# Kernel optimization log

Measured on AMD Instinct MI355X. Metric: run time of the kernel, lower is better.

The kernel has to match this reference:

```python
import jax, jax.numpy as jnp
import numpy as np

B, NC, H, GH = 64, 21, 32, 64  # batch, num_class, hidden spatial, geo spatial
DN = ('NCHW', 'OIHW', 'NCHW')


def conv2d(x, w, b, stride, pad):
    y = jax.lax.conv_general_dilated(x, w, (stride, stride), [(pad, pad), (pad, pad)], dimension_numbers=DN)
    return y + b[None, :, None, None]


def group_norm(x, scale, bias, groups=32, eps=1e-5):
    b, c, h, w = x.shape
    xg = x.reshape(b, groups, c // groups, h, w)
    mean = xg.mean(axis=(2, 3, 4), keepdims=True)
    var = xg.var(axis=(2, 3, 4), keepdims=True)
    xn = ((xg - mean) * jax.lax.rsqrt(var + eps)).reshape(b, c, h, w)
    return xn * scale[None, :, None, None] + bias[None, :, None, None]


def setup_inputs() -> dict:
    key = jax.random.key(0)
    ks = iter(jax.random.split(key, 64))
    rn = lambda shape, s=0.05: jax.random.normal(next(ks), shape, jnp.float32) * s
    inp = {
        'hidden_state': jnp.tanh(rn((B, 128, H, H), 1.0)),
        'delta_flow': rn((B, 2, H, H), 1.0),
        'mask': jax.random.uniform(next(ks), (B, 1, H, H), jnp.float32),
        'geo': rn((B, 8, GH, GH), 1.0),
        'obj_id': jax.random.randint(next(ks), (B,), 1, NC + 1),
        # geo_model
        'g1_w': rn((128, 8, 3, 3)), 'g1_b': rn((128,)),
        'g2_w': rn((64, 128, 3, 3)), 'g2_b': rn((64,)),
        # delta_flow_model
        'd1_w': rn((128, 2, 7, 7)), 'd1_b': rn((128,)),
        'd2_w': rn((64, 128, 3, 3)), 'd2_b': rn((64,)),
        # mask_model
        'm1_w': rn((64, 1, 3, 3)), 'm1_b': rn((64,)),
        'm2_w': rn((32, 64, 3, 3)), 'm2_b': rn((32,)),
        # conv_layers (conv + GroupNorm(32) x3, all stride 2)
        'c1_w': rn((128, 288, 3, 3)), 'c1_b': rn((128,)), 'gn1_s': jnp.ones((128,)), 'gn1_bb': jnp.zeros((128,)),
        'c2_w': rn((128, 128, 3, 3)), 'c2_b': rn((128,)), 'gn2_s': jnp.ones((128,)), 'gn2_bb': jnp.zeros((128,)),
        'c3_w': rn((128, 128, 3, 3)), 'c3_b': rn((128,)), 'gn3_s': jnp.ones((128,)), 'gn3_bb': jnp.zeros((128,)),
        # fc_layers
        'fc1_w': rn((1024, 2048)), 'fc1_b': rn((1024,)),
        'fc2_w': rn((256, 1024)), 'fc2_b': rn((256,)),
        # prediction heads (random instead of zero-init so grads are non-trivial)
        'rot_w': rn((6 * NC, 256)), 'rot_b': jnp.tile(jnp.array([1., 0., 0., 0., 1., 0.], jnp.float32), NC),
        'tr_w': rn((3 * NC, 256)), 'tr_b': rn((3 * NC,)),
    }
    return inp


def reference(hidden_state, delta_flow, mask, geo, obj_id,
              g1_w, g1_b, g2_w, g2_b, d1_w, d1_b, d2_w, d2_b, m1_w, m1_b, m2_w, m2_b,
              c1_w, c1_b, gn1_s, gn1_bb, c2_w, c2_b, gn2_s, gn2_bb, c3_w, c3_b, gn3_s, gn3_bb,
              fc1_w, fc1_b, fc2_w, fc2_b, rot_w, rot_b, tr_w, tr_b):
    relu = jax.nn.relu
    geo_enc = relu(conv2d(relu(conv2d(geo, g1_w, g1_b, 1, 1)), g2_w, g2_b, 2, 1))        # [B,64,32,32]
    df_enc = relu(conv2d(relu(conv2d(delta_flow, d1_w, d1_b, 1, 3)), d2_w, d2_b, 1, 1))  # [B,64,32,32]
    m_enc = relu(conv2d(relu(conv2d(mask, m1_w, m1_b, 1, 1)), m2_w, m2_b, 1, 1))         # [B,32,32,32]
    enc = jnp.concatenate([hidden_state, df_enc, m_enc, geo_enc], axis=1)                # [B,288,32,32]
    x = relu(group_norm(conv2d(enc, c1_w, c1_b, 2, 1), gn1_s, gn1_bb))                   # [B,128,16,16]
    x = relu(group_norm(conv2d(x, c2_w, c2_b, 2, 1), gn2_s, gn2_bb))                     # [B,128,8,8]
    x = relu(group_norm(conv2d(x, c3_w, c3_b, 2, 1), gn3_s, gn3_bb))                     # [B,128,4,4]
    x = x.reshape(x.shape[0], -1)                                                        # [B,2048]
    x = relu(x @ fc1_w.T + fc1_b)
    x = relu(x @ fc2_w.T + fc2_b)                                                        # [B,256]
    tr = (x @ tr_w.T + tr_b).reshape(-1, NC, 3)
    rot = (x @ rot_w.T + rot_b).reshape(-1, NC, 6)
    # torch.index_select(., dim=1, index=obj_id-1)[:, 0, :] -> uses obj_id[0]
    tr = jnp.take(tr, obj_id - 1, axis=1)[:, 0, :]
    rot = jnp.take(rot, obj_id - 1, axis=1)[:, 0, :]
    return (rot, tr)
```

## Files before the change

kernel.cpp:

```cpp
#include <hip/hip_runtime.h>
#include <hip/hip_bf16.h>

typedef __bf16 bf16x8 __attribute__((ext_vector_type(8)));
typedef __bf16 bf16x4 __attribute__((ext_vector_type(4)));
typedef float  f32x4  __attribute__((ext_vector_type(4)));

struct PackArgs {
    const float* src[11];
    __bf16* dst[11];
    int Cout[11], Cin[11], KHW[11], KW[11], Cinpad[11], Kpad[11], mode[11];
    int cum[12];
};

__device__ void pack_dev(const PackArgs& pa, int gidx)
{
    if (gidx >= pa.cum[11]) return;
    int s = 0;
    for (int i = 1; i <= 10; ++i) s += (gidx >= pa.cum[i]) ? 1 : 0;
    int l = gidx - pa.cum[s];
    int Kp = pa.Kpad[s];
    int co = l / Kp, k = l - co * Kp;
    float v = 0.f;
    if (co < pa.Cout[s]) {
        if (pa.mode[s] == 0) {
            int cip = pa.Cinpad[s];
            int tap = k / cip, ci = k - tap * cip;
            if (tap < pa.KHW[s] && ci < pa.Cin[s])
                v = pa.src[s][((long)co * pa.Cin[s] + ci) * pa.KHW[s] + tap];
        } else if (pa.mode[s] == 1) {
            int pix = k >> 7, c = k & 127;
            v = pa.src[s][(long)co * 2048 + c * 16 + pix];
        } else if (pa.mode[s] == 2) {
            v = pa.src[s][(long)co * Kp + k];
        } else {
            int kh = k >> 4, r = k & 15, kw = r >> 1, ci = r & 1;
            if (kh < 7 && kw < 7)
                v = pa.src[s][((long)(co * 2 + ci) * 7 + kh) * 7 + kw];
        }
    }
    pa.dst[s][l] = (__bf16)v;
}

__device__ void pad_nhwc8_dev(const float* __restrict__ in, __bf16* __restrict__ out,
                              int C, int log2HW, long idx)
{
    int c = idx & 7;
    long pixb = idx >> 3;
    long b = pixb >> log2HW;
    long pix = pixb & ((1 << log2HW) - 1);
    float v = 0.f;
    if (c < C) v = in[((b * C + c) << log2HW) + pix];
    out[idx] = (__bf16)v;
}

__device__ void pad_dflow_dev(const float* __restrict__ in, __bf16* __restrict__ out, int idx)
{
    if (idx >= 64 * 40 * 40 * 2) return;
    int c = idx & 1;
    int t = idx >> 1;
    int x = t % 40;
    int t2 = t / 40;
    int y = t2 % 40;
    int b = t2 / 40;
    int hi = y - 3, wi = x - 3;
    float v = 0.f;
    if ((unsigned)hi < 32u && (unsigned)wi < 32u)
        v = in[((long)(b * 2 + c) * 32 + hi) * 32 + wi];
    out[idx] = (__bf16)v;
}

__device__ void hid_dev(const float* __restrict__ h, __bf16* __restrict__ enc, int blk, int tid)
{
    __shared__ float t[32][65];
    int b = blk >> 6;
    int inner = blk & 63;
    int ct = inner & 3, pt = inner >> 2;
    int c0 = ct * 32, p0 = pt * 64;
    int cl = tid >> 6, pl = tid & 63;
#pragma unroll
    for (int i = 0; i < 8; ++i)
        t[cl + i * 4][pl] = h[((long)(b * 128 + c0 + cl + i * 4)) * 1024 + p0 + pl];
    __syncthreads();
    int cc = tid & 31, p2 = tid >> 5;
#pragma unroll
    for (int i = 0; i < 8; ++i)
        enc[((long)b * 1024 + p0 + p2 + i * 8) * 288 + c0 + cc] = (__bf16)t[cc][p2 + i * 8];
}

#define PACK_B 12544
#define GEOPAD_B 8192
#define DF_B 800
#define MASK_B 2048
#define HID_B 4096
#define ZERO_B 80
__global__ __launch_bounds__(256) void prep_kern(PackArgs pa,
    const float* __restrict__ geo, __bf16* __restrict__ geo_p,
    const float* __restrict__ dflow, __bf16* __restrict__ dflow_pp,
    const float* __restrict__ mask, __bf16* __restrict__ mask_p,
    const float* __restrict__ hidden, __bf16* __restrict__ enc,
    float* __restrict__ fc1acc, float* __restrict__ fc2acc)
{
    int blk = blockIdx.x, tid = threadIdx.x;
    if (blk < PACK_B) { pack_dev(pa, blk * 256 + tid); return; }
    blk -= PACK_B;
    if (blk < GEOPAD_B) { pad_nhwc8_dev(geo, geo_p, 8, 12, (long)blk * 256 + tid); return; }
    blk -= GEOPAD_B;
    if (blk < DF_B) { pad_dflow_dev(dflow, dflow_pp, blk * 256 + tid); return; }
    blk -= DF_B;
    if (blk < MASK_B) { pad_nhwc8_dev(mask, mask_p, 1, 10, (long)blk * 256 + tid); return; }
    blk -= MASK_B;
    if (blk < HID_B) { hid_dev(hidden, enc, blk, tid); return; }
    blk -= HID_B;
    long zi = (long)blk * 256 + tid;
    f32x4 z = {};
    if (zi < 16384) *(f32x4*)&fc1acc[zi * 4] = z;
    else { zi -= 16384; *(f32x4*)&fc2acc[zi * 4] = z; }
}

struct ConvGeom {
    int CinTot;
    int Hin, Win;
    int log2HWout, log2Wout;
    int stride, pad;
    int Kpad;
    int KHW;
    int Cout, CTOT, C0;
    int b0i, b0o;
};

template<int BM, int BN, int BK, int THREADS, int WMW, int WNW, int CINPAD, int KW, int MODE, bool OUTBF, bool RELU>
__device__ __forceinline__ void conv_dev2(char* __restrict__ smem_, int bx,
    const __bf16* __restrict__ in_, const __bf16* __restrict__ A,
    const float* __restrict__ bias, void* __restrict__ out_, const ConvGeom& g)
{
    constexpr int MEXT = BM / WMW;
    constexpr int NEXT = BN / WNW;
    constexpr int MFRAG = MEXT / 16;
    constexpr int NFRAG = NEXT / 16;
    constexpr int KROW = BK / 8;
    constexpr int SROWS = THREADS / KROW;
    constexpr int APASS = BM / SROWS;
    constexpr int BPASS = BN / SROWS;
    constexpr int LDK = BK + 8;

    auto As = reinterpret_cast<__bf16 (*)[LDK]>(smem_);
    auto Bs = reinterpret_cast<__bf16 (*)[LDK]>(smem_ + (size_t)BM * LDK * sizeof(__bf16));

    const int tid = threadIdx.x;
    const int ntile = bx * BN;
    const int lane = tid & 63, w = tid >> 6;
    const int wm = (w / WNW) * MEXT, wn = (w % WNW) * NEXT;
    const int lr = lane & 15, lk = (lane >> 4) * 8;
    const int srow = tid / KROW, scol = (tid % KROW) * 8;

    long nbase[BPASS]; int hi0a[BPASS], wi0a[BPASS];
#pragma unroll
    for (int j = 0; j < BPASS; ++j) {
        int n = ntile + j * SROWS + srow;
        int bb = g.b0i + (n >> g.log2HWout);
        int pix = n & ((1 << g.log2HWout) - 1);
        int ho = pix >> g.log2Wout, wo = pix & ((1 << g.log2Wout) - 1);
        hi0a[j] = ho * g.stride - g.pad;
        wi0a[j] = wo * g.stride - g.pad;
        nbase[j] = (((long)bb * g.Hin + hi0a[j]) * g.Win + wi0a[j]) * g.CinTot;
    }

    bf16x8 av[APASS], bv[BPASS];
    auto LOAD = [&](int k0) {
        int k = k0 + scol;
#pragma unroll
        for (int ja = 0; ja < APASS; ++ja)
            av[ja] = *(const bf16x8*)&A[(long)(ja * SROWS + srow) * g.Kpad + k];
        if (MODE == 1) {
            int q = k >> 3;
            int off = (q >> 1) * (g.Win * g.CinTot) + (q & 1) * 8;
#pragma unroll
            for (int j = 0; j < BPASS; ++j)
                bv[j] = *(const bf16x8*)&in_[nbase[j] + off];
        } else {
            int tap = k / CINPAD;
            int ci  = k - tap * CINPAD;
            int kh  = tap / KW;
            int kw  = tap - kh * KW;
            bool tv = tap < g.KHW;
            int off = (kh * g.Win + kw) * g.CinTot + ci;
#pragma unroll
            for (int j = 0; j < BPASS; ++j) {
                bf16x8 z = {};
                int hi = hi0a[j] + kh, wi = wi0a[j] + kw;
                if (tv && (unsigned)hi < (unsigned)g.Hin && (unsigned)wi < (unsigned)g.Win)
                    z = *(const bf16x8*)&in_[nbase[j] + off];
                bv[j] = z;
            }
        }
    };

    f32x4 acc[MFRAG][NFRAG] = {};
    LOAD(0);
    for (int k0 = 0;;) {
        if (k0) __syncthreads();
#pragma unroll
        for (int ja = 0; ja < APASS; ++ja)
            *(bf16x8*)&As[ja * SROWS + srow][scol] = av[ja];
#pragma unroll
        for (int j = 0; j < BPASS; ++j)
            *(bf16x8*)&Bs[j * SROWS + srow][scol] = bv[j];
        __syncthreads();
        int kn = k0 + BK;
        bool more = kn < g.Kpad;
        if (more) LOAD(kn);
#pragma unroll
        for (int kk = 0; kk < BK; kk += 32) {
            bf16x8 bfr[NFRAG], afr[MFRAG];
#pragma unroll
            for (int jn = 0; jn < NFRAG; ++jn)
                bfr[jn] = *(const bf16x8*)&Bs[wn + jn * 16 + lr][kk + lk];
#pragma unroll
            for (int i = 0; i < MFRAG; ++i)
                afr[i] = *(const bf16x8*)&As[wm + i * 16 + lr][kk + lk];
#pragma unroll
            for (int i = 0; i < MFRAG; ++i)
#pragma unroll
                for (int jn = 0; jn < NFRAG; ++jn)
                    acc[i][jn] = __builtin_amdgcn_mfma_f32_16x16x32_bf16(afr[i], bfr[jn], acc[i][jn], 0, 0, 0);
        }
        if (!more) break;
        k0 = kn;
    }

    const int HWm1 = (1 << g.log2HWout) - 1;
#pragma unroll
    for (int i = 0; i < MFRAG; ++i) {
        int co = wm + i * 16 + (lane >> 4) * 4;
        if (co >= g.Cout) continue;
        f32x4 bv4 = *(const f32x4*)&bias[co];
#pragma unroll
        for (int jn = 0; jn < NFRAG; ++jn) {
            int nn = ntile + wn + jn * 16 + lr;
            f32x4 v = acc[i][jn] + bv4;
            if (RELU) { v.x = fmaxf(v.x, 0.f); v.y = fmaxf(v.y, 0.f); v.z = fmaxf(v.z, 0.f); v.w = fmaxf(v.w, 0.f); }
            int ob = nn >> g.log2HWout, opix = nn & HWm1;
            long o = (((long)(g.b0o + ob) << g.log2HWout) + opix) * g.CTOT + g.C0 + co;
            if (OUTBF) {
                bf16x4 o4 = { (__bf16)v.x, (__bf16)v.y, (__bf16)v.z, (__bf16)v.w };
                *(bf16x4*)&((__bf16*)out_)[o] = o4;
            } else {
                *(f32x4*)&((float*)out_)[o] = v;
            }
        }
    }
}

template<int BM, int BN, int BK, int THREADS, int CINPAD, int KW, int MODE, bool OUTBF, bool RELU>
__device__ __forceinline__ void conv_dev(char* __restrict__ smem_, int bx,
    const __bf16* __restrict__ in_, const __bf16* __restrict__ A,
    const float* __restrict__ bias, void* __restrict__ out_, const ConvGeom& g)
{
    constexpr int WAVES = THREADS / 64;
    constexpr int WN = BN / 32;
    constexpr int WM = WAVES / WN;
    constexpr int MEXT = BM / WM;
    constexpr int MFRAG = MEXT / 16;
    constexpr int KROW = BK / 8;
    constexpr int SROWS = THREADS / KROW;
    constexpr int APASS = BM / SROWS;
    constexpr int BPASS = BN / SROWS;

    auto As = reinterpret_cast<__bf16 (*)[BK + 8]>(smem_);
    auto Bs = reinterpret_cast<__bf16 (*)[BK + 8]>(smem_ + (size_t)BM * (BK + 8) * sizeof(__bf16));

    const int tid = threadIdx.x;
    const int ntile = bx * BN;
    const int lane = tid & 63, w = tid >> 6;
    const int wm = (w / WN) * MEXT, wn = (w % WN) * 32;
    const int lr = lane & 15, lk = (lane >> 4) * 8;
    const int srow = tid / KROW, scol = (tid % KROW) * 8;

    long nbase[BPASS]; int hi0a[BPASS], wi0a[BPASS];
#pragma unroll
    for (int j = 0; j < BPASS; ++j) {
        int n = ntile + j * SROWS + srow;
        int bb = g.b0i + (n >> g.log2HWout);
        int pix = n & ((1 << g.log2HWout) - 1);
        int ho = pix >> g.log2Wout, wo = pix & ((1 << g.log2Wout) - 1);
        hi0a[j] = ho * g.stride - g.pad;
        wi0a[j] = wo * g.stride - g.pad;
        nbase[j] = (((long)bb * g.Hin + hi0a[j]) * g.Win + wi0a[j]) * g.CinTot;
    }

    bf16x8 av[APASS], bv[BPASS];
    auto LOAD = [&](int k0) {
        int k = k0 + scol;
#pragma unroll
        for (int ja = 0; ja < APASS; ++ja)
            av[ja] = *(const bf16x8*)&A[(long)(ja * SROWS + srow) * g.Kpad + k];
        if (MODE == 1) {
            int q = k >> 3;
            int off = (q >> 1) * (g.Win * g.CinTot) + (q & 1) * 8;
#pragma unroll
            for (int j = 0; j < BPASS; ++j)
                bv[j] = *(const bf16x8*)&in_[nbase[j] + off];
        } else {
            int tap = k / CINPAD;
            int ci  = k - tap * CINPAD;
            int kh  = tap / KW;
            int kw  = tap - kh * KW;
            bool tv = tap < g.KHW;
            int off = (kh * g.Win + kw) * g.CinTot + ci;
#pragma unroll
            for (int j = 0; j < BPASS; ++j) {
                bf16x8 z = {};
                int hi = hi0a[j] + kh, wi = wi0a[j] + kw;
                if (tv && (unsigned)hi < (unsigned)g.Hin && (unsigned)wi < (unsigned)g.Win)
                    z = *(const bf16x8*)&in_[nbase[j] + off];
                bv[j] = z;
            }
        }
    };

    f32x4 acc[MFRAG][2] = {};
    LOAD(0);
    for (int k0 = 0;;) {
        if (k0) __syncthreads();
#pragma unroll
        for (int ja = 0; ja < APASS; ++ja)
            *(bf16x8*)&As[ja * SROWS + srow][scol] = av[ja];
#pragma unroll
        for (int j = 0; j < BPASS; ++j)
            *(bf16x8*)&Bs[j * SROWS + srow][scol] = bv[j];
        __syncthreads();
        int kn = k0 + BK;
        bool more = kn < g.Kpad;
        if (more) LOAD(kn);
#pragma unroll
        for (int kk = 0; kk < BK; kk += 32) {
            bf16x8 bfr[2];
            bfr[0] = *(const bf16x8*)&Bs[wn + lr][kk + lk];
            bfr[1] = *(const bf16x8*)&Bs[wn + 16 + lr][kk + lk];
#pragma unroll
            for (int i = 0; i < MFRAG; ++i) {
                bf16x8 a = *(const bf16x8*)&As[wm + i * 16 + lr][kk + lk];
                acc[i][0] = __builtin_amdgcn_mfma_f32_16x16x32_bf16(a, bfr[0], acc[i][0], 0, 0, 0);
                acc[i][1] = __builtin_amdgcn_mfma_f32_16x16x32_bf16(a, bfr[1], acc[i][1], 0, 0, 0);
            }
        }
        if (!more) break;
        k0 = kn;
    }

    const int HWm1 = (1 << g.log2HWout) - 1;
#pragma unroll
    for (int i = 0; i < MFRAG; ++i) {
        int co = wm + i * 16 + (lane >> 4) * 4;
        if (co >= g.Cout) continue;
        f32x4 bv4 = *(const f32x4*)&bias[co];
#pragma unroll
        for (int jb = 0; jb < 2; ++jb) {
            int nn = ntile + wn + jb * 16 + lr;
            f32x4 v = acc[i][jb] + bv4;
            if (RELU) { v.x = fmaxf(v.x, 0.f); v.y = fmaxf(v.y, 0.f); v.z = fmaxf(v.z, 0.f); v.w = fmaxf(v.w, 0.f); }
            int ob = nn >> g.log2HWout, opix = nn & HWm1;
            long o = (((long)(g.b0o + ob) << g.log2HWout) + opix) * g.CTOT + g.C0 + co;
            if (OUTBF) {
                bf16x4 o4 = { (__bf16)v.x, (__bf16)v.y, (__bf16)v.z, (__bf16)v.w };
                *(bf16x4*)&((__bf16*)out_)[o] = o4;
            } else {
                *(f32x4*)&((float*)out_)[o] = v;
            }
        }
    }
}

template<int BM, int BN, int BK, int THREADS, int WMW, int WNW, int CINPAD, int KW, int MODE, bool OUTBF, bool RELU>
__global__ __launch_bounds__(THREADS) void conv_gemm2(
    const __bf16* __restrict__ in_, const __bf16* __restrict__ A,
    const float* __restrict__ bias, void* __restrict__ out_, ConvGeom g)
{
    __shared__ __attribute__((aligned(16))) char smem[(BM + BN) * (BK + 8) * 2];
    int mt = blockIdx.y * BM;
    ConvGeom gg = g;
    gg.C0 += mt;
    gg.Cout -= mt;
    conv_dev2<BM, BN, BK, THREADS, WMW, WNW, CINPAD, KW, MODE, OUTBF, RELU>(
        smem, blockIdx.x, in_, A + (long)mt * g.Kpad, bias + mt, out_, gg);
}

template<int BM, int BN, int BK, int THREADS, int WMW, int WNW, int CINPAD, int KW, int PPB>
__global__ __launch_bounds__(THREADS) void conv_gn_kern(
    const __bf16* __restrict__ in_, const __bf16* __restrict__ A,
    const float* __restrict__ bias, const float* __restrict__ gns,
    const float* __restrict__ gnb, __bf16* __restrict__ out_, ConvGeom g)
{
    constexpr int MEXT = BM / WMW;
    constexpr int NEXT = BN / WNW;
    constexpr int MFRAG = MEXT / 16;
    constexpr int NFRAG = NEXT / 16;
    constexpr int KROW = BK / 8;
    constexpr int SROWS = THREADS / KROW;
    constexpr int APASS = BM / SROWS;
    constexpr int BPASS = BN / SROWS;
    constexpr int LDK = BK + 8;

    __shared__ __attribute__((aligned(16))) char smem_[(BM + BN) * (BK + 8) * 2];
    auto As = reinterpret_cast<__bf16 (*)[LDK]>(smem_);
    auto Bs = reinterpret_cast<__bf16 (*)[LDK]>(smem_ + (size_t)BM * LDK * sizeof(__bf16));
    static_assert((size_t)BN * (BM + 4) * 4 <= (size_t)(BM + BN) * (BK + 8) * 2, "smf fits");

    const int tid = threadIdx.x;
    const int mt = blockIdx.y * BM;
    const __bf16* Ap = A + (long)mt * g.Kpad;
    const int C0 = g.C0 + mt;
    const int ntile = blockIdx.x * BN;
    const int lane = tid & 63, w = tid >> 6;
    const int wm = (w / WNW) * MEXT, wn = (w % WNW) * NEXT;
    const int lr = lane & 15, lk = (lane >> 4) * 8;
    const int srow = tid / KROW, scol = (tid % KROW) * 8;

    long nbase[BPASS]; int hi0a[BPASS], wi0a[BPASS];
#pragma unroll
    for (int j = 0; j < BPASS; ++j) {
        int n = ntile + j * SROWS + srow;
        int bb = g.b0i + (n >> g.log2HWout);
        int pix = n & ((1 << g.log2HWout) - 1);
        int ho = pix >> g.log2Wout, wo = pix & ((1 << g.log2Wout) - 1);
        hi0a[j] = ho * g.stride - g.pad;
        wi0a[j] = wo * g.stride - g.pad;
        nbase[j] = (((long)bb * g.Hin + hi0a[j]) * g.Win + wi0a[j]) * g.CinTot;
    }

    bf16x8 av[APASS], bv[BPASS];
    auto LOAD = [&](int k0) {
        int k = k0 + scol;
#pragma unroll
        for (int ja = 0; ja < APASS; ++ja)
            av[ja] = *(const bf16x8*)&Ap[(long)(ja * SROWS + srow) * g.Kpad + k];
        int tap = k / CINPAD;
        int ci  = k - tap * CINPAD;
        int kh  = tap / KW;
        int kw  = tap - kh * KW;
        bool tv = tap < g.KHW;
        int off = (kh * g.Win + kw) * g.CinTot + ci;
#pragma unroll
        for (int j = 0; j < BPASS; ++j) {
            bf16x8 z = {};
            int hi = hi0a[j] + kh, wi = wi0a[j] + kw;
            if (tv && (unsigned)hi < (unsigned)g.Hin && (unsigned)wi < (unsigned)g.Win)
                z = *(const bf16x8*)&in_[nbase[j] + off];
            bv[j] = z;
        }
    };

    f32x4 acc[MFRAG][NFRAG] = {};
    LOAD(0);
    for (int k0 = 0;;) {
        if (k0) __syncthreads();
#pragma unroll
        for (int ja = 0; ja < APASS; ++ja)
            *(bf16x8*)&As[ja * SROWS + srow][scol] = av[ja];
#pragma unroll
        for (int j = 0; j < BPASS; ++j)
            *(bf16x8*)&Bs[j * SROWS + srow][scol] = bv[j];
        __syncthreads();
        int kn = k0 + BK;
        bool more = kn < g.Kpad;
        if (more) LOAD(kn);
#pragma unroll
        for (int kk = 0; kk < BK; kk += 32) {
            bf16x8 bfr[NFRAG], afr[MFRAG];
#pragma unroll
            for (int jn = 0; jn < NFRAG; ++jn)
                bfr[jn] = *(const bf16x8*)&Bs[wn + jn * 16 + lr][kk + lk];
#pragma unroll
            for (int i = 0; i < MFRAG; ++i)
                afr[i] = *(const bf16x8*)&As[wm + i * 16 + lr][kk + lk];
#pragma unroll
            for (int i = 0; i < MFRAG; ++i)
#pragma unroll
                for (int jn = 0; jn < NFRAG; ++jn)
                    acc[i][jn] = __builtin_amdgcn_mfma_f32_16x16x32_bf16(afr[i], bfr[jn], acc[i][jn], 0, 0, 0);
        }
        if (!more) break;
        k0 = kn;
    }

    __syncthreads();
    auto smf = reinterpret_cast<float (*)[BM + 4]>(smem_);
#pragma unroll
    for (int i = 0; i < MFRAG; ++i) {
        int m = wm + i * 16 + (lane >> 4) * 4;
        f32x4 bv4 = *(const f32x4*)&bias[C0 + m];
#pragma unroll
        for (int jn = 0; jn < NFRAG; ++jn) {
            int n = wn + jn * 16 + lr;
            *(f32x4*)&smf[n][m] = acc[i][jn] + bv4;
        }
    }
    __syncthreads();

    constexpr int NSETS = (BN / PPB) * (BM / 4);
    constexpr int TPS = THREADS / NSETS;
    constexpr int PPT = PPB / TPS;
    const int set = tid / TPS, part = tid % TPS;
    const int bit = set / (BM / 4);
    const int grp = set % (BM / 4);
    const int m0 = grp * 4;
    float sum = 0.f, sq = 0.f;
#pragma unroll
    for (int p = 0; p < PPT; ++p) {
        int nl = bit * PPB + part + p * TPS;
        f32x4 v = *(const f32x4*)&smf[nl][m0];
        sum += v.x + v.y + v.z + v.w;
        sq  += v.x * v.x + v.y * v.y + v.z * v.z + v.w * v.w;
    }
#pragma unroll
    for (int off = TPS >> 1; off > 0; off >>= 1) {
        sum += __shfl_xor(sum, off);
        sq  += __shfl_xor(sq, off);
    }
    const float len = (float)(PPB * 4);
    float mean = sum / len;
    float var  = sq / len - mean * mean;
    float rstd = rsqrtf(fmaxf(var, 0.f) + 1e-5f);
    f32x4 s4 = *(const f32x4*)&gns[C0 + m0];
    f32x4 b4 = *(const f32x4*)&gnb[C0 + m0];
    const int HWm1 = (1 << g.log2HWout) - 1;
#pragma unroll
    for (int p = 0; p < PPT; ++p) {
        int nl = bit * PPB + part + p * TPS;
        f32x4 v = *(const f32x4*)&smf[nl][m0];
        f32x4 r;
        r.x = fmaxf((v.x - mean) * rstd * s4.x + b4.x, 0.f);
        r.y = fmaxf((v.y - mean) * rstd * s4.y + b4.y, 0.f);
        r.z = fmaxf((v.z - mean) * rstd * s4.z + b4.z, 0.f);
        r.w = fmaxf((v.w - mean) * rstd * s4.w + b4.w, 0.f);
        int n = ntile + nl;
        int ob = n >> g.log2HWout, opix = n & HWm1;
        long o = (((long)(g.b0o + ob) << g.log2HWout) + opix) * g.CTOT + C0 + m0;
        bf16x4 o4 = { (__bf16)r.x, (__bf16)r.y, (__bf16)r.z, (__bf16)r.w };
        *(bf16x4*)&out_[o] = o4;
    }
}

__global__ __launch_bounds__(512) void branch1_kern(
    const __bf16* __restrict__ geo_p, const __bf16* __restrict__ wg1, const float* __restrict__ g1_b, __bf16* __restrict__ g1out,
    const __bf16* __restrict__ dflow_pp, const __bf16* __restrict__ wd1, const float* __restrict__ d1_b, __bf16* __restrict__ d1out,
    const __bf16* __restrict__ mask_p, const __bf16* __restrict__ wm1, const float* __restrict__ m1_b, __bf16* __restrict__ m1out,
    ConvGeom gg1, ConvGeom gd1, ConvGeom gm1)
{
    __shared__ __attribute__((aligned(16))) char smem[27648];
    int x = blockIdx.x;
    if (x < 2048)
        conv_dev<128, 128, 32, 512, 8, 3, 0, true, true>(smem, x, geo_p, wg1, g1_b, g1out, gg1);
    else if (x < 2560)
        conv_dev<128, 128, 32, 512, 8, 7, 1, true, true>(smem, x - 2048, dflow_pp, wd1, d1_b, d1out, gd1);
    else
        conv_dev<64, 128, 64, 512, 8, 3, 0, true, true>(smem, x - 2560, mask_p, wm1, m1_b, m1out, gm1);
}

__global__ __launch_bounds__(256) void branch2_kern(
    const __bf16* __restrict__ g1out, const __bf16* __restrict__ wg2, const float* __restrict__ g2_b,
    const __bf16* __restrict__ d1out, const __bf16* __restrict__ wd2, const float* __restrict__ d2_b,
    const __bf16* __restrict__ m1out, const __bf16* __restrict__ wm2, const float* __restrict__ m2_b,
    __bf16* __restrict__ enc, ConvGeom gg2, ConvGeom gd2, ConvGeom gm2)
{
    __shared__ __attribute__((aligned(16))) char smem[(64 + 128) * (64 + 8) * 2];
    int x = blockIdx.x;
    int sec = x % 3, bx = x / 3;
    if (sec == 0)
        conv_dev2<64, 128, 64, 256, 1, 4, 128, 3, 0, true, true>(smem, bx, g1out, wg2, g2_b, enc, gg2);
    else if (sec == 1)
        conv_dev2<64, 128, 64, 256, 1, 4, 128, 3, 0, true, true>(smem, bx, d1out, wd2, d2_b, enc, gd2);
    else
        conv_dev2<64, 128, 64, 256, 1, 4, 64, 3, 0, true, true>(smem, bx, m1out, wm2, m2_b, enc, gm2);
}

__global__ __launch_bounds__(256) void fc1_splitk(
    const __bf16* __restrict__ A, const __bf16* __restrict__ B,
    float* __restrict__ outacc)
{
    __shared__ __attribute__((aligned(16))) __bf16 As[64][40];
    __shared__ __attribute__((aligned(16))) __bf16 Bs[64][40];
    const int tid = threadIdx.x;
    const int mtile = blockIdx.y * 64;
    const int kbase = blockIdx.x * 512;
    const int lane = tid & 63, w = tid >> 6;
    const int wm = (w >> 1) * 32, wn = (w & 1) * 32;
    const int lr = lane & 15, lk = (lane >> 4) * 8;
    const int srow = tid >> 2, soff = (tid & 3) * 8;

    f32x4 acc00 = {}, acc01 = {}, acc10 = {}, acc11 = {};
    for (int k0 = 0; k0 < 512; k0 += 32) {
        *(bf16x8*)&As[srow][soff] = *(const bf16x8*)&A[(long)(mtile + srow) * 2048 + kbase + k0 + soff];
        *(bf16x8*)&Bs[srow][soff] = *(const bf16x8*)&B[(long)srow * 2048 + kbase + k0 + soff];
        __syncthreads();
        bf16x8 a0 = *(const bf16x8*)&As[wm + lr][lk];
        bf16x8 a1 = *(const bf16x8*)&As[wm + 16 + lr][lk];
        bf16x8 b0f = *(const bf16x8*)&Bs[wn + lr][lk];
        bf16x8 b1f = *(const bf16x8*)&Bs[wn + 16 + lr][lk];
        acc00 = __builtin_amdgcn_mfma_f32_16x16x32_bf16(a0, b0f, acc00, 0, 0, 0);
        acc01 = __builtin_amdgcn_mfma_f32_16x16x32_bf16(a0, b1f, acc01, 0, 0, 0);
        acc10 = __builtin_amdgcn_mfma_f32_16x16x32_bf16(a1, b0f, acc10, 0, 0, 0);
        acc11 = __builtin_amdgcn_mfma_f32_16x16x32_bf16(a1, b1f, acc11, 0, 0, 0);
        __syncthreads();
    }
    f32x4 accs[2][2] = { { acc00, acc01 }, { acc10, acc11 } };
#pragma unroll
    for (int mi = 0; mi < 2; ++mi) {
        int co0 = mtile + wm + mi * 16 + (lane >> 4) * 4;
#pragma unroll
        for (int ni = 0; ni < 2; ++ni) {
            int nn = wn + ni * 16 + lr;
            f32x4 v = accs[mi][ni];
            float* dst = &outacc[(long)nn * 1024 + co0];
            atomicAdd(dst + 0, v.x);
            atomicAdd(dst + 1, v.y);
            atomicAdd(dst + 2, v.z);
            atomicAdd(dst + 3, v.w);
        }
    }
}

__global__ __launch_bounds__(256) void fc2_splitk(
    const __bf16* __restrict__ A, const float* __restrict__ Bacc,
    const float* __restrict__ bb, float* __restrict__ outacc)
{
    __shared__ __attribute__((aligned(16))) __bf16 As[64][40];
    __shared__ __attribute__((aligned(16))) __bf16 Bs[64][40];
    const int tid = threadIdx.x;
    const int mtile = blockIdx.y * 64;
    const int kbase = blockIdx.x * 256;
    const int lane = tid & 63, w = tid >> 6;
    const int wm = (w >> 1) * 32, wn = (w & 1) * 32;
    const int lr = lane & 15, lk = (lane >> 4) * 8;
    const int srow = tid >> 2, soff = (tid & 3) * 8;

    f32x4 acc00 = {}, acc01 = {}, acc10 = {}, acc11 = {};
    for (int k0 = 0; k0 < 256; k0 += 32) {
        int k = kbase + k0 + soff;
        *(bf16x8*)&As[srow][soff] = *(const bf16x8*)&A[(long)(mtile + srow) * 1024 + k];
        f32x4 lo = *(const f32x4*)&Bacc[(long)srow * 1024 + k];
        f32x4 hi = *(const f32x4*)&Bacc[(long)srow * 1024 + k + 4];
        f32x4 blo = *(const f32x4*)&bb[k];
        f32x4 bhi = *(const f32x4*)&bb[k + 4];
        bf16x8 bvv;
        bvv[0] = (__bf16)fmaxf(lo.x + blo.x, 0.f);
        bvv[1] = (__bf16)fmaxf(lo.y + blo.y, 0.f);
        bvv[2] = (__bf16)fmaxf(lo.z + blo.z, 0.f);
        bvv[3] = (__bf16)fmaxf(lo.w + blo.w, 0.f);
        bvv[4] = (__bf16)fmaxf(hi.x + bhi.x, 0.f);
        bvv[5] = (__bf16)fmaxf(hi.y + bhi.y, 0.f);
        bvv[6] = (__bf16)fmaxf(hi.z + bhi.z, 0.f);
        bvv[7] = (__bf16)fmaxf(hi.w + bhi.w, 0.f);
        *(bf16x8*)&Bs[srow][soff] = bvv;
        __syncthreads();
        bf16x8 a0 = *(const bf16x8*)&As[wm + lr][lk];
        bf16x8 a1 = *(const bf16x8*)&As[wm + 16 + lr][lk];
        bf16x8 b0f = *(const bf16x8*)&Bs[wn + lr][lk];
        bf16x8 b1f = *(const bf16x8*)&Bs[wn + 16 + lr][lk];
        acc00 = __builtin_amdgcn_mfma_f32_16x16x32_bf16(a0, b0f, acc00, 0, 0, 0);
        acc01 = __builtin_amdgcn_mfma_f32_16x16x32_bf16(a0, b1f, acc01, 0, 0, 0);
        acc10 = __builtin_amdgcn_mfma_f32_16x16x32_bf16(a1, b0f, acc10, 0, 0, 0);
        acc11 = __builtin_amdgcn_mfma_f32_16x16x32_bf16(a1, b1f, acc11, 0, 0, 0);
        __syncthreads();
    }
    f32x4 accs[2][2] = { { acc00, acc01 }, { acc10, acc11 } };
#pragma unroll
    for (int mi = 0; mi < 2; ++mi) {
        int co0 = mtile + wm + mi * 16 + (lane >> 4) * 4;
#pragma unroll
        for (int ni = 0; ni < 2; ++ni) {
            int nn = wn + ni * 16 + lr;
            f32x4 v = accs[mi][ni];
            float* dst = &outacc[(long)nn * 256 + co0];
            atomicAdd(dst + 0, v.x);
            atomicAdd(dst + 1, v.y);
            atomicAdd(dst + 2, v.z);
            atomicAdd(dst + 3, v.w);
        }
    }
}

__global__ void gn_nhwc(const float* __restrict__ in, const float* __restrict__ s,
                        const float* __restrict__ bi, __bf16* __restrict__ out,
                        int C, int HW)
{
    int b = blockIdx.x >> 5, g = blockIdx.x & 31;
    int tid = threadIdx.x, nt = blockDim.x;
    const float* p = in + (long)b * HW * C + g * 4;
    float sum = 0.f, sq = 0.f;
    for (int i = tid; i < HW; i += nt) {
        f32x4 v = *(const f32x4*)&p[(long)i * C];
        sum += v.x + v.y + v.z + v.w;
        sq  += v.x * v.x + v.y * v.y + v.z * v.z + v.w * v.w;
    }
    __shared__ float rs[256], rq[256];
    rs[tid] = sum; rq[tid] = sq; __syncthreads();
    for (int off = nt >> 1; off > 0; off >>= 1) {
        if (tid < off) { rs[tid] += rs[tid + off]; rq[tid] += rq[tid + off]; }
        __syncthreads();
    }
    int len = HW * 4;
    float mean = rs[0] / len;
    float var  = rq[0] / len - mean * mean;
    float rstd = rsqrtf(fmaxf(var, 0.f) + 1e-5f);
    f32x4 s4 = *(const f32x4*)&s[g * 4];
    f32x4 b4 = *(const f32x4*)&bi[g * 4];
    __bf16* q = out + (long)b * HW * C + g * 4;
    for (int i = tid; i < HW; i += nt) {
        f32x4 v = *(const f32x4*)&p[(long)i * C];
        f32x4 r;
        r.x = fmaxf((v.x - mean) * rstd * s4.x + b4.x, 0.f);
        r.y = fmaxf((v.y - mean) * rstd * s4.y + b4.y, 0.f);
        r.z = fmaxf((v.z - mean) * rstd * s4.z + b4.z, 0.f);
        r.w = fmaxf((v.w - mean) * rstd * s4.w + b4.w, 0.f);
        bf16x4 o4 = { (__bf16)r.x, (__bf16)r.y, (__bf16)r.z, (__bf16)r.w };
        *(bf16x4*)&q[(long)i * C] = o4;
    }
}

__global__ void head_kern(const float* __restrict__ x, const float* __restrict__ fb,
                          const float* __restrict__ rw, const float* __restrict__ rb,
                          const float* __restrict__ tw, const float* __restrict__ tb,
                          const int* __restrict__ obj, float* __restrict__ out)
{
    int t = threadIdx.x;
    if (t >= 64 * 9) return;
    int b = t / 9, k = t % 9;
    int j = obj[0] - 1;
    const float* xr = x + (long)b * 256;
    float acc;
    const float* wr;
    if (k < 6) { wr = rw + (long)(j * 6 + k) * 256; acc = rb[j * 6 + k]; }
    else       { wr = tw + (long)(j * 3 + (k - 6)) * 256; acc = tb[j * 3 + (k - 6)]; }
    for (int i = 0; i < 256; ++i) {
        float xv = fmaxf(xr[i] + fb[i], 0.f);
        acc = fmaf(xv, wr[i], acc);
    }
    if (k < 6) out[b * 6 + k] = acc;
    else       out[384 + b * 3 + (k - 6)] = acc;
}

extern "C" void kernel_launch(void* const* d_in, const int* in_sizes, int n_in,
                              void* d_out, int out_size, void* d_ws, size_t ws_size,
                              hipStream_t stream)
{
    const float* hidden = (const float*)d_in[0];
    const float* dflow  = (const float*)d_in[1];
    const float* mask   = (const float*)d_in[2];
    const float* geo    = (const float*)d_in[3];
    const int*   obj    = (const int*)d_in[4];
    const float* g1_w = (const float*)d_in[5],  *g1_b = (const float*)d_in[6];
    const float* g2_w = (const float*)d_in[7],  *g2_b = (const float*)d_in[8];
    const float* d1_w = (const float*)d_in[9],  *d1_b = (const float*)d_in[10];
    const float* d2_w = (const float*)d_in[11], *d2_b = (const float*)d_in[12];
    const float* m1_w = (const float*)d_in[13], *m1_b = (const float*)d_in[14];
    const float* m2_w = (const float*)d_in[15], *m2_b = (const float*)d_in[16];
    const float* c1_w = (const float*)d_in[17], *c1_b = (const float*)d_in[18];
    const float* gn1_s = (const float*)d_in[19], *gn1_bb = (const float*)d_in[20];
    const float* c2_w = (const float*)d_in[21], *c2_b = (const float*)d_in[22];
    const float* gn2_s = (const float*)d_in[23], *gn2_bb = (const float*)d_in[24];
    const float* c3_w = (const float*)d_in[25], *c3_b = (const float*)d_in[26];
    const float* gn3_s = (const float*)d_in[27], *gn3_bb = (const float*)d_in[28];
    const float* fc1_w = (const float*)d_in[29], *fc1_b = (const float*)d_in[30];
    const float* fc2_w = (const float*)d_in[31], *fc2_b = (const float*)d_in[32];
    const float* rot_w = (const float*)d_in[33], *rot_b = (const float*)d_in[34];
    const float* tr_w  = (const float*)d_in[35], *tr_b  = (const float*)d_in[36];

    char* ws = (char*)d_ws;
    __bf16* enc = (__bf16*)ws;
    char* W = ws + 37748736;
    __bf16* wg1  = (__bf16*)(W + 0);
    __bf16* wd1  = (__bf16*)(W + 24576);
    __bf16* wm1  = (__bf16*)(W + 57344);
    __bf16* wg2  = (__bf16*)(W + 73728);
    __bf16* wd2  = (__bf16*)(W + 221184);
    __bf16* wm2  = (__bf16*)(W + 368640);
    __bf16* wc1  = (__bf16*)(W + 442368);
    __bf16* wc2  = (__bf16*)(W + 1114112);
    __bf16* wc3  = (__bf16*)(W + 1409024);
    __bf16* wfc1 = (__bf16*)(W + 1703936);
    __bf16* wfc2 = (__bf16*)(W + 5898240);
    __bf16* geo_p    = (__bf16*)(ws + 44179456);
    __bf16* dflow_pp = (__bf16*)(ws + 48373760);
    __bf16* mask_p   = (__bf16*)(ws + 48783360);
    __bf16* g1out    = (__bf16*)(ws + 49831936);
    __bf16* d1out    = (__bf16*)(ws + 116940800);
    __bf16* m1out    = (__bf16*)(ws + 133718016);
    float*  c1raw    = (float*)(ws + 142106624);
    __bf16* x1       = (__bf16*)(ws + 150495232);
    __bf16* x2       = (__bf16*)(ws + 156786688);
    __bf16* x3       = (__bf16*)(ws + 158359552);
    float*  fc1acc   = (float*)(ws + 158621696);
    float*  fc2acc   = (float*)(ws + 158883840);

    {
        PackArgs pa;
        const float* srcs[11] = { g1_w, d1_w, m1_w, g2_w, d2_w, m2_w, c1_w, c2_w, c3_w, fc1_w, fc2_w };
        __bf16* dsts[11] = { wg1, wd1, wm1, wg2, wd2, wm2, wc1, wc2, wc3, wfc1, wfc2 };
        int Co[11]  = { 128, 128, 64, 64, 64, 32, 128, 128, 128, 1024, 256 };
        int Ci[11]  = { 8, 2, 1, 128, 128, 64, 288, 128, 128, 0, 0 };
        int KH[11]  = { 9, 49, 9, 9, 9, 9, 9, 9, 9, 0, 0 };
        int KWn[11] = { 3, 7, 3, 3, 3, 3, 3, 3, 3, 0, 0 };
        int Cp[11]  = { 8, 8, 8, 128, 128, 64, 288, 128, 128, 0, 0 };
        int Kp[11]  = { 96, 128, 128, 1152, 1152, 576, 2624, 1152, 1152, 2048, 1024 };
        int Mp[11]  = { 128, 128, 64, 64, 64, 64, 128, 128, 128, 1024, 256 };
        int Md[11]  = { 0, 3, 0, 0, 0, 0, 0, 0, 0, 1, 2 };
        int c = 0; pa.cum[0] = 0;
        for (int i = 0; i < 11; ++i) {
            pa.src[i] = srcs[i]; pa.dst[i] = dsts[i];
            pa.Cout[i] = Co[i]; pa.Cin[i] = Ci[i]; pa.KHW[i] = KH[i]; pa.KW[i] = KWn[i];
            pa.Cinpad[i] = Cp[i]; pa.Kpad[i] = Kp[i]; pa.mode[i] = Md[i];
            c += Mp[i] * Kp[i]; pa.cum[i + 1] = c;
        }
        int total_blocks = PACK_B + GEOPAD_B + DF_B + MASK_B + HID_B + ZERO_B;
        prep_kern<<<dim3(total_blocks), 256, 0, stream>>>(pa, geo, geo_p, dflow, dflow_pp,
                                                          mask, mask_p, hidden, enc,
                                                          fc1acc, fc2acc);
    }

    {
        ConvGeom gg1 = { 8, 64, 64, 12, 6, 1, 1, 96, 9, 128, 128, 0, 0, 0 };
        ConvGeom gd1 = { 2, 40, 40, 10, 5, 1, 0, 128, 49, 128, 128, 0, 0, 0 };
        ConvGeom gm1 = { 8, 32, 32, 10, 5, 1, 1, 128, 9, 64, 64, 0, 0, 0 };
        branch1_kern<<<dim3(3072), 512, 0, stream>>>(geo_p, wg1, g1_b, g1out,
                                                     dflow_pp, wd1, d1_b, d1out,
                                                     mask_p, wm1, m1_b, m1out,
                                                     gg1, gd1, gm1);
    }
    {
        ConvGeom gg2 = { 128, 64, 64, 10, 5, 2, 1, 1152, 9, 64, 288, 224, 0, 0 };
        ConvGeom gd2 = { 128, 32, 32, 10, 5, 1, 1, 1152, 9, 64, 288, 128, 0, 0 };
        ConvGeom gm2 = { 64, 32, 32, 10, 5, 1, 1, 576, 9, 32, 288, 192, 0, 0 };
        branch2_kern<<<dim3(1536), 256, 0, stream>>>(g1out, wg2, g2_b,
                                                     d1out, wd2, d2_b,
                                                     m1out, wm2, m2_b,
                                                     enc, gg2, gd2, gm2);
    }

    {
        ConvGeom gc1 = { 288, 32, 32, 8, 4, 2, 1, 2624, 9, 128, 128, 0, 0, 0 };
        conv_gemm2<64, 128, 64, 256, 1, 4, 288, 3, 0, false, false><<<dim3(128, 2), 256, 0, stream>>>(enc, wc1, c1_b, c1raw, gc1);
    }
    gn_nhwc<<<dim3(2048), 256, 0, stream>>>(c1raw, gn1_s, gn1_bb, x1, 128, 256);

    {
        ConvGeom gc2 = { 128, 16, 16, 6, 3, 2, 1, 1152, 9, 128, 128, 0, 0, 0 };
        conv_gn_kern<64, 64, 64, 256, 2, 2, 128, 3, 64><<<dim3(64, 2), 256, 0, stream>>>(
            x1, wc2, c2_b, gn2_s, gn2_bb, x2, gc2);
    }
    {
        ConvGeom gc3 = { 128, 8, 8, 4, 2, 2, 1, 1152, 9, 128, 128, 0, 0, 0 };
        conv_gn_kern<64, 64, 64, 256, 2, 2, 128, 3, 16><<<dim3(16, 2), 256, 0, stream>>>(
            x2, wc3, c3_b, gn3_s, gn3_bb, x3, gc3);
    }

    fc1_splitk<<<dim3(4, 16), 256, 0, stream>>>(wfc1, x3, fc1acc);
    fc2_splitk<<<dim3(4, 4), 256, 0, stream>>>(wfc2, fc1acc, fc1_b, fc2acc);

    head_kern<<<dim3(1), 576, 0, stream>>>(fc2acc, fc2_b, rot_w, rot_b, tr_w, tr_b, obj, (float*)d_out);
}
```

Before: 242.0 us.

## Move weight packing and hidden transpose into branch kernels to overlap work

The prep kernel now packs only the branch-1 weights (the first 144 blocks). The remaining weight packing moves into extra blocks of branch1_kern, and the hidden-state transpose into enc moves into extra blocks of branch2_kern, so this memory-bound work overlaps with the compute-bound conv blocks instead of sitting on the critical path. The head kernel is also parallelised from one block with a serial 256-long dot product to 64 blocks using wave-wide shuffle reductions. The risk is that the added blocks compete with the conv blocks for CUs and bandwidth, and that the split pack offset (36864) must match the cumulative sizes exactly.

```diff
diff --git a/kernel.cpp b/kernel.cpp
--- a/kernel.cpp
+++ b/kernel.cpp
@@ -69,9 +69,10 @@
     out[idx] = (__bf16)v;
 }
 
-__device__ void hid_dev(const float* __restrict__ h, __bf16* __restrict__ enc, int blk, int tid)
-{
-    __shared__ float t[32][65];
+__device__ void hid_dev(char* smem, const float* __restrict__ h,
+                        __bf16* __restrict__ enc, int blk, int tid)
+{
+    auto t = reinterpret_cast<float (*)[65]>(smem);
     int b = blk >> 6;
     int inner = blk & 63;
     int ct = inner & 3, pt = inner >> 2;
@@ -87,17 +88,15 @@
         enc[((long)b * 1024 + p0 + p2 + i * 8) * 288 + c0 + cc] = (__bf16)t[cc][p2 + i * 8];
 }
 
-#define PACK_B 12544
+#define PACK_B 144
 #define GEOPAD_B 8192
 #define DF_B 800
 #define MASK_B 2048
-#define HID_B 4096
 #define ZERO_B 80
 __global__ __launch_bounds__(256) void prep_kern(PackArgs pa,
     const float* __restrict__ geo, __bf16* __restrict__ geo_p,
     const float* __restrict__ dflow, __bf16* __restrict__ dflow_pp,
     const float* __restrict__ mask, __bf16* __restrict__ mask_p,
-    const float* __restrict__ hidden, __bf16* __restrict__ enc,
     float* __restrict__ fc1acc, float* __restrict__ fc2acc)
 {
     int blk = blockIdx.x, tid = threadIdx.x;
@@ -109,8 +108,6 @@
     blk -= DF_B;
     if (blk < MASK_B) { pad_nhwc8_dev(mask, mask_p, 1, 10, (long)blk * 256 + tid); return; }
     blk -= MASK_B;
-    if (blk < HID_B) { hid_dev(hidden, enc, blk, tid); return; }
-    blk -= HID_B;
     long zi = (long)blk * 256 + tid;
     f32x4 z = {};
     if (zi < 16384) *(f32x4*)&fc1acc[zi * 4] = z;
@@ -541,11 +538,13 @@
     }
 }
 
+#define B1_CONV 3072
+#define B1_PACK 6200
 __global__ __launch_bounds__(512) void branch1_kern(
     const __bf16* __restrict__ geo_p, const __bf16* __restrict__ wg1, const float* __restrict__ g1_b, __bf16* __restrict__ g1out,
     const __bf16* __restrict__ dflow_pp, const __bf16* __restrict__ wd1, const float* __restrict__ d1_b, __bf16* __restrict__ d1out,
     const __bf16* __restrict__ mask_p, const __bf16* __restrict__ wm1, const float* __restrict__ m1_b, __bf16* __restrict__ m1out,
-    ConvGeom gg1, ConvGeom gd1, ConvGeom gm1)
+    PackArgs pa, ConvGeom gg1, ConvGeom gd1, ConvGeom gm1)
 {
     __shared__ __attribute__((aligned(16))) char smem[27648];
     int x = blockIdx.x;
@@ -553,18 +552,24 @@
         conv_dev<128, 128, 32, 512, 8, 3, 0, true, true>(smem, x, geo_p, wg1, g1_b, g1out, gg1);
     else if (x < 2560)
         conv_dev<128, 128, 32, 512, 8, 7, 1, true, true>(smem, x - 2048, dflow_pp, wd1, d1_b, d1out, gd1);
+    else if (x < B1_CONV)
+        conv_dev<64, 128, 64, 512, 8, 3, 0, true, true>(smem, x - 2560, mask_p, wm1, m1_b, m1out, gm1);
     else
-        conv_dev<64, 128, 64, 512, 8, 3, 0, true, true>(smem, x - 2560, mask_p, wm1, m1_b, m1out, gm1);
-}
-
+        pack_dev(pa, 36864 + (x - B1_CONV) * 512 + threadIdx.x);
+}
+
+#define B2_CONV 1536
+#define B2_HID 4096
 __global__ __launch_bounds__(256) void branch2_kern(
     const __bf16* __restrict__ g1out, const __bf16* __restrict__ wg2, const float* __restrict__ g2_b,
     const __bf16* __restrict__ d1out, const __bf16* __restrict__ wd2, const float* __restrict__ d2_b,
     const __bf16* __restrict__ m1out, const __bf16* __restrict__ wm2, const float* __restrict__ m2_b,
-    __bf16* __restrict__ enc, ConvGeom gg2, ConvGeom gd2, ConvGeom gm2)
+    const float* __restrict__ hidden, __bf16* __restrict__ enc,
+    ConvGeom gg2, ConvGeom gd2, ConvGeom gm2)
 {
     __shared__ __attribute__((aligned(16))) char smem[(64 + 128) * (64 + 8) * 2];
     int x = blockIdx.x;
+    if (x >= B2_CONV) { hid_dev(smem, hidden, enc, x - B2_CONV, threadIdx.x); return; }
     int sec = x % 3, bx = x / 3;
     if (sec == 0)
         conv_dev2<64, 128, 64, 256, 1, 4, 128, 3, 0, true, true>(smem, bx, g1out, wg2, g2_b, enc, gg2);
@@ -718,26 +723,35 @@
     }
 }
 
-__global__ void head_kern(const float* __restrict__ x, const float* __restrict__ fb,
-                          const float* __restrict__ rw, const float* __restrict__ rb,
-                          const float* __restrict__ tw, const float* __restrict__ tb,
-                          const int* __restrict__ obj, float* __restrict__ out)
-{
-    int t = threadIdx.x;
-    if (t >= 64 * 9) return;
-    int b = t / 9, k = t % 9;
+__global__ __launch_bounds__(576) void head_kern(
+    const float* __restrict__ x, const float* __restrict__ fb,
+    const float* __restrict__ rw, const float* __restrict__ rb,
+    const float* __restrict__ tw, const float* __restrict__ tb,
+    const int* __restrict__ obj, float* __restrict__ out)
+{
+    int b = blockIdx.x;
+    int k = threadIdx.x >> 6;
+    int lane = threadIdx.x & 63;
     int j = obj[0] - 1;
     const float* xr = x + (long)b * 256;
-    float acc;
     const float* wr;
-    if (k < 6) { wr = rw + (long)(j * 6 + k) * 256; acc = rb[j * 6 + k]; }
-    else       { wr = tw + (long)(j * 3 + (k - 6)) * 256; acc = tb[j * 3 + (k - 6)]; }
-    for (int i = 0; i < 256; ++i) {
+    float bias0;
+    if (k < 6) { wr = rw + (long)(j * 6 + k) * 256; bias0 = rb[j * 6 + k]; }
+    else       { wr = tw + (long)(j * 3 + (k - 6)) * 256; bias0 = tb[j * 3 + (k - 6)]; }
+    float acc = 0.f;
+#pragma unroll
+    for (int p = 0; p < 4; ++p) {
+        int i = lane + p * 64;
         float xv = fmaxf(xr[i] + fb[i], 0.f);
         acc = fmaf(xv, wr[i], acc);
     }
-    if (k < 6) out[b * 6 + k] = acc;
-    else       out[384 + b * 3 + (k - 6)] = acc;
+#pragma unroll
+    for (int off = 32; off > 0; off >>= 1) acc += __shfl_down(acc, off);
+    if (lane == 0) {
+        float r = acc + bias0;
+        if (k < 6) out[b * 6 + k] = r;
+        else       out[384 + b * 3 + (k - 6)] = r;
+    }
 }
 
 extern "C" void kernel_launch(void* const* d_in, const int* in_sizes, int n_in,
@@ -793,8 +807,8 @@
     float*  fc1acc   = (float*)(ws + 158621696);
     float*  fc2acc   = (float*)(ws + 158883840);
 
+    PackArgs pa;
     {
-        PackArgs pa;
         const float* srcs[11] = { g1_w, d1_w, m1_w, g2_w, d2_w, m2_w, c1_w, c2_w, c3_w, fc1_w, fc2_w };
         __bf16* dsts[11] = { wg1, wd1, wm1, wg2, wd2, wm2, wc1, wc2, wc3, wfc1, wfc2 };
         int Co[11]  = { 128, 128, 64, 64, 64, 32, 128, 128, 128, 1024, 256 };
@@ -812,29 +826,31 @@
             pa.Cinpad[i] = Cp[i]; pa.Kpad[i] = Kp[i]; pa.mode[i] = Md[i];
             c += Mp[i] * Kp[i]; pa.cum[i + 1] = c;
         }
-        int total_blocks = PACK_B + GEOPAD_B + DF_B + MASK_B + HID_B + ZERO_B;
+    }
+
+    {
+        int total_blocks = PACK_B + GEOPAD_B + DF_B + MASK_B + ZERO_B;
         prep_kern<<<dim3(total_blocks), 256, 0, stream>>>(pa, geo, geo_p, dflow, dflow_pp,
-                                                          mask, mask_p, hidden, enc,
-                                                          fc1acc, fc2acc);
+                                                          mask, mask_p, fc1acc, fc2acc);
     }
 
     {
         ConvGeom gg1 = { 8, 64, 64, 12, 6, 1, 1, 96, 9, 128, 128, 0, 0, 0 };
         ConvGeom gd1 = { 2, 40, 40, 10, 5, 1, 0, 128, 49, 128, 128, 0, 0, 0 };
         ConvGeom gm1 = { 8, 32, 32, 10, 5, 1, 1, 128, 9, 64, 64, 0, 0, 0 };
-        branch1_kern<<<dim3(3072), 512, 0, stream>>>(geo_p, wg1, g1_b, g1out,
-                                                     dflow_pp, wd1, d1_b, d1out,
-                                                     mask_p, wm1, m1_b, m1out,
-                                                     gg1, gd1, gm1);
+        branch1_kern<<<dim3(B1_CONV + B1_PACK), 512, 0, stream>>>(geo_p, wg1, g1_b, g1out,
+                                                                  dflow_pp, wd1, d1_b, d1out,
+                                                                  mask_p, wm1, m1_b, m1out,
+                                                                  pa, gg1, gd1, gm1);
     }
     {
         ConvGeom gg2 = { 128, 64, 64, 10, 5, 2, 1, 1152, 9, 64, 288, 224, 0, 0 };
         ConvGeom gd2 = { 128, 32, 32, 10, 5, 1, 1, 1152, 9, 64, 288, 128, 0, 0 };
         ConvGeom gm2 = { 64, 32, 32, 10, 5, 1, 1, 576, 9, 32, 288, 192, 0, 0 };
-        branch2_kern<<<dim3(1536), 256, 0, stream>>>(g1out, wg2, g2_b,
-                                                     d1out, wd2, d2_b,
-                                                     m1out, wm2, m2_b,
-                                                     enc, gg2, gd2, gm2);
+        branch2_kern<<<dim3(B2_CONV + B2_HID), 256, 0, stream>>>(g1out, wg2, g2_b,
+                                                                 d1out, wd2, d2_b,
+                                                                 m1out, wm2, m2_b,
+                                                                 hidden, enc, gg2, gd2, gm2);
     }
 
     {
@@ -857,5 +873,5 @@
     fc1_splitk<<<dim3(4, 16), 256, 0, stream>>>(wfc1, x3, fc1acc);
     fc2_splitk<<<dim3(4, 4), 256, 0, stream>>>(wfc2, fc1acc, fc1_b, fc2acc);
 
-    head_kern<<<dim3(1), 576, 0, stream>>>(fc2acc, fc2_b, rot_w, rot_b, tr_w, tr_b, obj, (float*)d_out);
-}
+    head_kern<<<dim3(64), 576, 0, stream>>>(fc2acc, fc2_b, rot_w, rot_b, tr_w, tr_b, obj, (float*)d_out);
+}
```

Result: faster. 216.5 us (-10.6%).
